# Performance work log

Hardware: AMD Instinct MI355X
Metric: run time of the kernel (lower is better)

The kernel has to match this reference:

```python
import jax, jax.numpy as jnp
import numpy as np

B, N = 16384, 4096

def setup_inputs() -> dict:
    key = jax.random.key(0)
    k1, k2 = jax.random.split(key)
    # ~1/3 zeros so the mask is nontrivial
    x = jax.random.randint(k1, (B, N), 0, 3).astype(jnp.float32)
    t = jnp.zeros((), dtype=jnp.float32)  # unused time scalar
    f = jax.random.normal(k2, (1,), dtype=jnp.float32)  # learned scalar param
    return {"t": t, "x": x, "f": f}

def reference(t, x, f):
    # Vectorized form of the per-row python loop:
    #   for each row i: y[i, mask] = f / sum(f over mask)
    mask = x != 0                                   # [B, N] bool
    fb = jnp.broadcast_to(f, x.shape)               # f.expand(x.shape)
    row_sum = jnp.sum(jnp.where(mask, fb, 0.0), axis=1, keepdims=True)  # [B, 1]
    # rows with no nonzero entries stay zero (torch skips them via numel check)
    safe = jnp.where(row_sum != 0.0, row_sum, 1.0)
    y = jnp.where(mask, fb / safe, 0.0)             # [B, N]
    return y
```

## Files before the change

kernel.cpp:

```cpp
#include <hip/hip_runtime.h>


#define NCOL 4096
#define NV4  (NCOL / 4)
#define BLK  256
#define PER_THREAD 4

__global__ __launch_bounds__(BLK, 4)
void filt_norm_kernel(const float* __restrict__ x,
                      const float* __restrict__ f,
                      float* __restrict__ y,
                      int nrows) {
    __shared__ int   wsum[BLK / 64];
    __shared__ float sval;

    const int tid = threadIdx.x;
    const float fv = f[0];

    for (int row = blockIdx.x; row < nrows; row += gridDim.x) {
        const float4* __restrict__ xr = (const float4*)x + (size_t)row * NV4;
        float4*       __restrict__ yr = (float4*)y       + (size_t)row * NV4;

        float4 v[PER_THREAD];
        #pragma unroll
        for (int k = 0; k < PER_THREAD; ++k)
            v[k] = xr[tid + k * BLK];

        int c = 0;
        #pragma unroll
        for (int k = 0; k < PER_THREAD; ++k) {
            c += (v[k].x != 0.0f);
            c += (v[k].y != 0.0f);
            c += (v[k].z != 0.0f);
            c += (v[k].w != 0.0f);
        }

        #pragma unroll
        for (int off = 32; off > 0; off >>= 1)
            c += __shfl_down(c, off);
        if ((tid & 63) == 0) wsum[tid >> 6] = c;
        __syncthreads();
        if (tid == 0) {
            int cnt = wsum[0] + wsum[1] + wsum[2] + wsum[3];
            float rs = fv * (float)cnt;
            sval = fv / ((rs != 0.0f) ? rs : 1.0f);
        }
        __syncthreads();
        const float val = sval;

        #pragma unroll
        for (int k = 0; k < PER_THREAD; ++k) {
            float4 o;
            o.x = (v[k].x != 0.0f) ? val : 0.0f;
            o.y = (v[k].y != 0.0f) ? val : 0.0f;
            o.z = (v[k].z != 0.0f) ? val : 0.0f;
            o.w = (v[k].w != 0.0f) ? val : 0.0f;
            yr[tid + k * BLK] = o;
        }
    }
}

extern "C" void kernel_launch(void* const* d_in, const int* in_sizes, int n_in,
                              void* d_out, int out_size, void* d_ws, size_t ws_size,
                              hipStream_t stream) {
    const float* x = (const float*)d_in[1];
    const float* f = (const float*)d_in[2];
    float*       y = (float*)d_out;
    const int nrows = in_sizes[1] / NCOL;

    const int grid = 2048;
    filt_norm_kernel<<<grid, BLK, 0, stream>>>(x, f, y, nrows);
}
```

Measured before the change: 101.0 us.

## Assign one wavefront per row with bitmask and nontemporal loads/stores

Each 64-lane wavefront now processes a whole row, reducing the count with a popcount and xor-shuffles instead of a block-wide shared-memory reduction with two barriers. The nonzero pattern is packed into a 64-bit register mask rather than keeping loaded values live. Loads and stores use nontemporal hints to avoid cache pollution, and the persistent grid-stride loop is replaced by a grid sized to the rows. This aims to remove synchronization and improve streaming bandwidth, at the cost of losing the persistent-grid scheduling.

Result: faster. 91.35 us (median of 2 runs) (-9.5%).

```diff
diff --git a/kernel.cpp b/kernel.cpp
--- a/kernel.cpp
+++ b/kernel.cpp
@@ -1,62 +1,56 @@
 #include <hip/hip_runtime.h>
+#include <cstdint>
 
 
 #define NCOL 4096
 #define NV4  (NCOL / 4)
 #define BLK  256
-#define PER_THREAD 4
+#define WPB  4
 
-__global__ __launch_bounds__(BLK, 4)
+typedef float f4 __attribute__((ext_vector_type(4)));
+
+__global__ __launch_bounds__(BLK)
 void filt_norm_kernel(const float* __restrict__ x,
                       const float* __restrict__ f,
                       float* __restrict__ y,
                       int nrows) {
-    __shared__ int   wsum[BLK / 64];
-    __shared__ float sval;
+    const int lane = threadIdx.x & 63;
+    const int wid  = threadIdx.x >> 6;
+    const int row  = blockIdx.x * WPB + wid;
+    if (row >= nrows) return;
 
-    const int tid = threadIdx.x;
     const float fv = f[0];
+    const f4* __restrict__ xr = (const f4*)x + (size_t)row * NV4;
+    f4*       __restrict__ yr = (f4*)y       + (size_t)row * NV4;
 
-    for (int row = blockIdx.x; row < nrows; row += gridDim.x) {
-        const float4* __restrict__ xr = (const float4*)x + (size_t)row * NV4;
-        float4*       __restrict__ yr = (float4*)y       + (size_t)row * NV4;
+    uint64_t mask = 0;
+    #pragma unroll
+    for (int k = 0; k < 16; ++k) {
+        f4 v = __builtin_nontemporal_load(xr + lane + k * 64);
+        uint64_t m = 0;
+        m |= (v.x != 0.0f) ? 1ull : 0ull;
+        m |= (v.y != 0.0f) ? 2ull : 0ull;
+        m |= (v.z != 0.0f) ? 4ull : 0ull;
+        m |= (v.w != 0.0f) ? 8ull : 0ull;
+        mask |= m << (k * 4);
+    }
 
-        float4 v[PER_THREAD];
-        #pragma unroll
-        for (int k = 0; k < PER_THREAD; ++k)
-            v[k] = xr[tid + k * BLK];
+    int c = __popcll(mask);
+    #pragma unroll
+    for (int off = 32; off > 0; off >>= 1)
+        c += __shfl_xor(c, off);
 
-        int c = 0;
-        #pragma unroll
-        for (int k = 0; k < PER_THREAD; ++k) {
-            c += (v[k].x != 0.0f);
-            c += (v[k].y != 0.0f);
-            c += (v[k].z != 0.0f);
-            c += (v[k].w != 0.0f);
-        }
+    const float rs  = fv * (float)c;
+    const float val = fv / ((rs != 0.0f) ? rs : 1.0f);
 
-        #pragma unroll
-        for (int off = 32; off > 0; off >>= 1)
-            c += __shfl_down(c, off);
-        if ((tid & 63) == 0) wsum[tid >> 6] = c;
-        __syncthreads();
-        if (tid == 0) {
-            int cnt = wsum[0] + wsum[1] + wsum[2] + wsum[3];
-            float rs = fv * (float)cnt;
-            sval = fv / ((rs != 0.0f) ? rs : 1.0f);
-        }
-        __syncthreads();
-        const float val = sval;
-
-        #pragma unroll
-        for (int k = 0; k < PER_THREAD; ++k) {
-            float4 o;
-            o.x = (v[k].x != 0.0f) ? val : 0.0f;
-            o.y = (v[k].y != 0.0f) ? val : 0.0f;
-            o.z = (v[k].z != 0.0f) ? val : 0.0f;
-            o.w = (v[k].w != 0.0f) ? val : 0.0f;
-            yr[tid + k * BLK] = o;
-        }
+    #pragma unroll
+    for (int k = 0; k < 16; ++k) {
+        f4 o;
+        o.x = ((mask >> (k * 4 + 0)) & 1ull) ? val : 0.0f;
+        o.y = ((mask >> (k * 4 + 1)) & 1ull) ? val : 0.0f;
+        o.z = ((mask >> (k * 4 + 2)) & 1ull) ? val : 0.0f;
+        o.w = ((mask >> (k * 4 + 3)) & 1ull) ? val : 0.0f;
+        __builtin_nontemporal_store(o, yr + lane + k * 64);
     }
 }
 
@@ -68,6 +62,6 @@
     float*       y = (float*)d_out;
     const int nrows = in_sizes[1] / NCOL;
 
-    const int grid = 2048;
+    const int grid = (nrows + WPB - 1) / WPB;
     filt_norm_kernel<<<grid, BLK, 0, stream>>>(x, f, y, nrows);
 }
```
